# Performance work log

Measured on AMD Instinct MI355X. Metric: run time of the kernel, lower is better.

Reference implementation:

```python
import jax, jax.numpy as jnp
import numpy as np

VEC_DIM = 64
RANK = 2


def setup_inputs() -> dict:
    key = jax.random.key(0)
    kg, km, kp = jax.random.split(key, 3)
    grid = jax.random.normal(kg, (193, 193, VEC_DIM), dtype=jnp.float32)
    # nn.init.uniform_(M.weight, -0.5, 0.5)
    M_weight = jax.random.uniform(km, (VEC_DIM, VEC_DIM), minval=-0.5, maxval=0.5, dtype=jnp.float32)
    # nn.init.uniform_(P, -0.1, 0.1)
    P = jax.random.uniform(kp, (VEC_DIM, VEC_DIM), minval=-0.1, maxval=0.1, dtype=jnp.float32)
    return {"grid": grid, "M_weight": M_weight, "P": P}


def reference(grid, M_weight, P):
    H, W, m = grid.shape
    # periods1[i,j] = periods2[i,j] = i*m + j + 2
    periods = (jnp.arange(m, dtype=jnp.float32)[:, None] * m
               + jnp.arange(m, dtype=jnp.float32)[None, :] + 2.0)  # [m, m]

    # ---- window extraction: linear mode (step=1), rank_mode='drop', rank_op='avg' ----
    nH = H - RANK + 1
    nW = W - RANK + 1
    win_sum = jax.lax.reduce_window(grid, 0.0, jax.lax.add,
                                    (RANK, RANK, 1), (1, 1, 1), 'VALID')  # [nH, nW, m]
    x_win = (win_sum / float(RANK * RANK)).reshape(nH * nW, m)  # [B, m]

    # ---- map through M (nn.Linear, no bias): y = x @ W^T ----
    x = x_win @ M_weight.T  # [B, m]

    # ---- phi_table gather: phi[k1,k2] = cos(2*pi*k1/periods) * cos(2*pi*k2/periods) ----
    two_pi = jnp.float32(2.0 * np.pi)
    k1s = jnp.arange(nH, dtype=jnp.float32)
    k2s = jnp.arange(nW, dtype=jnp.float32)
    cos1 = jnp.cos(two_pi * k1s[:, None, None] / periods)  # [nH, m, m]
    cos2 = jnp.cos(two_pi * k2s[:, None, None] / periods)  # [nW, m, m]
    phi = (cos1[:, None, :, :] * cos2[None, :, :, :]).reshape(nH * nW, m, m)  # [B, m, m]

    # ---- Nk = einsum('bj,ij,bij->bi', x, P, phi) ----
    Nk = jnp.einsum('bj,ij,bij->bi', x, P, phi)  # [B, m]
    return Nk
```

## Files before the change

kernel.cpp:

```cpp
#include <hip/hip_runtime.h>
#include <math.h>

#define NH 192
#define NW 192
#define Wt 193
#define TG 24
#define NTILE (TG*TG)
#define TILE_SZ 4096
#define TBLK 3072

__device__ __forceinline__ float cos_rev(float num, float den) {
    float rev = num * __builtin_amdgcn_rcpf(den);
    rev = __builtin_amdgcn_fractf(rev);
    return __builtin_amdgcn_cosf(rev);
}

__global__ __launch_bounds__(256) void k_prep(const float* __restrict__ grid,
                                              const float* __restrict__ Mw,
                                              const float* __restrict__ P,
                                              float* __restrict__ Cz,
                                              float* __restrict__ CP1,
                                              float* __restrict__ xt) {
    __shared__ float Ms[64 * 64];
    __shared__ float win[64 * 68];
    int bx = blockIdx.x;
    int t = threadIdx.x;

    if (bx < TBLK) {
        int idx = bx * 256 + t;
        int r  = idx & 3;
        int i  = (idx >> 2) & 63;
        int kg = (idx >> 8) % 48;
        int j  = idx / 12288;
        int k  = kg * 4 + r;
        Cz[idx] = cos_rev((float)k, (float)(i * 64 + j + 2));
        int i2 = idx & 63;
        int k2 = (idx >> 6) % 192;
        int j2 = idx / 12288;
        int t2 = i2 * 64 + j2;
        CP1[idx] = cos_rev((float)k2, (float)(t2 + 2)) * P[t2];
        return;
    }

    int bb = bx - TBLK;
    int k1g = bb % TG, k2g = bb / TG;

    #pragma unroll
    for (int r = 0; r < 4; ++r) {
        int e = r * 256 + t;
        ((float4*)Ms)[e] = ((const float4*)Mw)[e];
    }

    {
        int c = t & 63, pq = t >> 6;
        const float* gb = grid + ((size_t)(k1g * 8) * Wt + k2g * 8) * 64;
        #pragma unroll
        for (int r = 0; r < 16; ++r) {
            int p = pq * 16 + r;
            int l1 = p >> 3, l2 = p & 7;
            const float* g0 = gb + ((size_t)l1 * Wt + l2) * 64;
            float s = g0[c] + g0[64 + c] + g0[Wt * 64 + c] + g0[Wt * 64 + 64 + c];
            win[p * 68 + c] = 0.25f * s;
        }
    }
    __syncthreads();

    int p = t & 63, jq = t >> 6;
    float4 wv[16];
    #pragma unroll
    for (int q = 0; q < 16; ++q) wv[q] = *(const float4*)&win[p * 68 + 4 * q];

    float* xb = xt + (size_t)(k1g * TG + k2g) * TILE_SZ;
    #pragma unroll
    for (int r = 0; r < 16; ++r) {
        int j = jq * 16 + r;
        float acc = 0.f;
        #pragma unroll
        for (int q = 0; q < 16; ++q) {
            float4 mv = *(const float4*)&Ms[j * 64 + 4 * q];
            acc += wv[q].x * mv.x + wv[q].y * mv.y + wv[q].z * mv.z + wv[q].w * mv.w;
        }
        xb[(size_t)j * 64 + p] = acc;
    }
}

__global__ __launch_bounds__(512) void k_main(const float* __restrict__ xt,
                                              const float* __restrict__ Cz,
                                              const float* __restrict__ CP1,
                                              float* __restrict__ out) {
    __shared__ float4 cs[2048];
    __shared__ float4 c1s[2048];
    int bx = blockIdx.x;
    int xcd = bx & 7, q = bx >> 3;
    int k1g = (xcd & 1) * 12 + (q % 12);
    int k2g = (xcd >> 1) * 6 + (q / 12);
    int t = threadIdx.x;
    int lane = t & 63;
    int w = __builtin_amdgcn_readfirstlane(t >> 6);
    int k1 = k1g * 8 + w;

    const float4* Cz4 = (const float4*)Cz;
    const float4* CP4 = (const float4*)CP1;
    const float*  xb  = xt + (size_t)(k1g * TG + k2g) * TILE_SZ + w * 8;
    const float*  c1f = (const float*)c1s;
    int kgb = k2g * 2;

    float acc[8];
    #pragma unroll
    for (int l2 = 0; l2 < 8; ++l2) acc[l2] = 0.f;

    for (int jc = 0; jc < 4; ++jc) {
        __syncthreads();
        #pragma unroll
        for (int r = 0; r < 4; ++r) {
            int e = r * 512 + t;
            int jj = e >> 7;
            cs[e]  = Cz4[(size_t)((jc * 16 + jj) * 48 + kgb + ((e >> 6) & 1)) * 64 + (e & 63)];
            c1s[e] = CP4[(size_t)(jc * 16 + jj) * 3072 + k1g * 128 + (e & 127)];
        }
        __syncthreads();

        #pragma unroll 4
        for (int jj = 0; jj < 16; ++jj) {
            int j = jc * 16 + jj;
            float  c1 = c1f[jj * 512 + w * 64 + lane];
            float4 v0 = cs[jj * 128 + lane];
            float4 v1 = cs[jj * 128 + 64 + lane];
            const float4* xj = (const float4*)(xb + (size_t)j * 64);
            float4 x0 = xj[0];
            float4 x1 = xj[1];
            float c2f[8] = {v0.x, v0.y, v0.z, v0.w, v1.x, v1.y, v1.z, v1.w};
            float xs[8]  = {x0.x, x0.y, x0.z, x0.w, x1.x, x1.y, x1.z, x1.w};
            #pragma unroll
            for (int l2 = 0; l2 < 8; ++l2)
                acc[l2] += xs[l2] * (c1 * c2f[l2]);
        }
    }

    size_t ob = ((size_t)k1 * NW + k2g * 8) * 64 + lane;
    #pragma unroll
    for (int l2 = 0; l2 < 8; ++l2)
        out[ob + (size_t)l2 * 64] = acc[l2];
}

extern "C" void kernel_launch(void* const* d_in, const int* in_sizes, int n_in,
                              void* d_out, int out_size, void* d_ws, size_t ws_size,
                              hipStream_t stream) {
    const float* grid = (const float*)d_in[0];
    const float* Mw   = (const float*)d_in[1];
    const float* P    = (const float*)d_in[2];
    float* out = (float*)d_out;

    float* Cz  = (float*)d_ws;
    float* CP1 = Cz + 786432;
    float* xt  = CP1 + 786432;

    k_prep<<<TBLK + NTILE, 256, 0, stream>>>(grid, Mw, P, Cz, CP1, xt);
    k_main<<<NTILE, 512, 0, stream>>>(xt, Cz, CP1, out);
}
```

Measured before the change: 101.1 us.

## Use 4x4 register tiles and direct-to-LDS loads in main kernel

```diff
diff --git a/kernel.cpp b/kernel.cpp
--- a/kernel.cpp
+++ b/kernel.cpp
@@ -33,12 +33,10 @@
         int kg = (idx >> 8) % 48;
         int j  = idx / 12288;
         int k  = kg * 4 + r;
-        Cz[idx] = cos_rev((float)k, (float)(i * 64 + j + 2));
-        int i2 = idx & 63;
-        int k2 = (idx >> 6) % 192;
-        int j2 = idx / 12288;
-        int t2 = i2 * 64 + j2;
-        CP1[idx] = cos_rev((float)k2, (float)(t2 + 2)) * P[t2];
+        int t2 = i * 64 + j;
+        float c = cos_rev((float)k, (float)(t2 + 2));
+        Cz[idx]  = c;
+        CP1[idx] = c * P[t2];
         return;
     }
 
@@ -84,63 +82,82 @@
     }
 }
 
-__global__ __launch_bounds__(512) void k_main(const float* __restrict__ xt,
+__global__ __launch_bounds__(256) void k_main(const float* __restrict__ xt,
                                               const float* __restrict__ Cz,
                                               const float* __restrict__ CP1,
                                               float* __restrict__ out) {
-    __shared__ float4 cs[2048];
-    __shared__ float4 c1s[2048];
+    __shared__ float4 ls[2048];
     int bx = blockIdx.x;
     int xcd = bx & 7, q = bx >> 3;
     int k1g = (xcd & 1) * 12 + (q % 12);
     int k2g = (xcd >> 1) * 6 + (q / 12);
     int t = threadIdx.x;
     int lane = t & 63;
-    int w = __builtin_amdgcn_readfirstlane(t >> 6);
-    int k1 = k1g * 8 + w;
+    int w  = __builtin_amdgcn_readfirstlane(t >> 6);
+    int h1 = w & 1, h2 = w >> 1;
 
     const float4* Cz4 = (const float4*)Cz;
     const float4* CP4 = (const float4*)CP1;
-    const float*  xb  = xt + (size_t)(k1g * TG + k2g) * TILE_SZ + w * 8;
-    const float*  c1f = (const float*)c1s;
-    int kgb = k2g * 2;
+    const float*  xb  = xt + (size_t)(k1g * TG + k2g) * TILE_SZ + h1 * 32 + h2 * 4;
+    int c1base = k1g * 2;
+    int c2base = k2g * 2;
 
-    float acc[8];
+    float4 acc[4];
     #pragma unroll
-    for (int l2 = 0; l2 < 8; ++l2) acc[l2] = 0.f;
+    for (int a = 0; a < 4; ++a) acc[a] = (float4){0.f, 0.f, 0.f, 0.f};
 
-    for (int jc = 0; jc < 4; ++jc) {
+    for (int jc = 0; jc < 8; ++jc) {
         __syncthreads();
         #pragma unroll
-        for (int r = 0; r < 4; ++r) {
-            int e = r * 512 + t;
-            int jj = e >> 7;
-            cs[e]  = Cz4[(size_t)((jc * 16 + jj) * 48 + kgb + ((e >> 6) & 1)) * 64 + (e & 63)];
-            c1s[e] = CP4[(size_t)(jc * 16 + jj) * 3072 + k1g * 128 + (e & 127)];
+        for (int r = 0; r < 8; ++r) {
+            int e = r * 256 + t;
+            const float4* src;
+            if (r < 4) {
+                int jj = e >> 7, g = (e >> 6) & 1, i = e & 63;
+                src = CP4 + ((size_t)((jc * 8 + jj) * 48 + c1base + g) * 64 + i);
+            } else {
+                int e2 = e - 1024;
+                int jj = e2 >> 7, g = (e2 >> 6) & 1, i = e2 & 63;
+                src = Cz4 + ((size_t)((jc * 8 + jj) * 48 + c2base + g) * 64 + i);
+            }
+            __builtin_amdgcn_global_load_lds(
+                (const __attribute__((address_space(1))) unsigned int*)src,
+                (__attribute__((address_space(3))) unsigned int*)&ls[e], 16, 0, 0);
         }
         __syncthreads();
 
-        #pragma unroll 4
-        for (int jj = 0; jj < 16; ++jj) {
-            int j = jc * 16 + jj;
-            float  c1 = c1f[jj * 512 + w * 64 + lane];
-            float4 v0 = cs[jj * 128 + lane];
-            float4 v1 = cs[jj * 128 + 64 + lane];
+        #pragma unroll
+        for (int jj = 0; jj < 8; ++jj) {
+            int j = jc * 8 + jj;
+            float4 A = ls[(jj * 2 + h1) * 64 + lane];
+            float4 B = ls[1024 + (jj * 2 + h2) * 64 + lane];
             const float4* xj = (const float4*)(xb + (size_t)j * 64);
             float4 x0 = xj[0];
-            float4 x1 = xj[1];
-            float c2f[8] = {v0.x, v0.y, v0.z, v0.w, v1.x, v1.y, v1.z, v1.w};
-            float xs[8]  = {x0.x, x0.y, x0.z, x0.w, x1.x, x1.y, x1.z, x1.w};
+            float4 x1 = xj[2];
+            float4 x2 = xj[4];
+            float4 x3 = xj[6];
+            float Af[4] = {A.x, A.y, A.z, A.w};
+            float4 xs[4] = {x0, x1, x2, x3};
             #pragma unroll
-            for (int l2 = 0; l2 < 8; ++l2)
-                acc[l2] += xs[l2] * (c1 * c2f[l2]);
+            for (int a = 0; a < 4; ++a) {
+                acc[a].x += xs[a].x * (Af[a] * B.x);
+                acc[a].y += xs[a].y * (Af[a] * B.y);
+                acc[a].z += xs[a].z * (Af[a] * B.z);
+                acc[a].w += xs[a].w * (Af[a] * B.w);
+            }
         }
     }
 
-    size_t ob = ((size_t)k1 * NW + k2g * 8) * 64 + lane;
+    int k1b = k1g * 8 + h1 * 4;
+    int k2b = k2g * 8 + h2 * 4;
     #pragma unroll
-    for (int l2 = 0; l2 < 8; ++l2)
-        out[ob + (size_t)l2 * 64] = acc[l2];
+    for (int a = 0; a < 4; ++a) {
+        size_t ob = ((size_t)(k1b + a) * NW + k2b) * 64 + lane;
+        out[ob]           = acc[a].x;
+        out[ob + 64]      = acc[a].y;
+        out[ob + 128]     = acc[a].z;
+        out[ob + 192]     = acc[a].w;
+    }
 }
 
 extern "C" void kernel_launch(void* const* d_in, const int* in_sizes, int n_in,
@@ -156,5 +173,5 @@
     float* xt  = CP1 + 786432;
 
     k_prep<<<TBLK + NTILE, 256, 0, stream>>>(grid, Mw, P, Cz, CP1, xt);
-    k_main<<<NTILE, 512, 0, stream>>>(xt, Cz, CP1, out);
+    k_main<<<NTILE, 256, 0, stream>>>(xt, Cz, CP1, out);
 }
```

New measurement: 108.5 us. 1.07x slower.
